# Optimization experiments

Measured on AMD Instinct MI355X. Metric: run time of the kernel, lower is better.

## Reference

```python
import jax, jax.numpy as jnp
import numpy as np

N_NODES = 50000
E0, E1 = 500000, 300000
D = 64  # node_embedding_size == h_feats == edge_embedding_sizes[i]


def _mlp(x, w0, b0, w1, b1, w2, b2):
    # Linear -> ReLU -> Linear -> ReLU -> Linear (nodes_in / edges_in stacks)
    h = jax.nn.relu(x @ w0 + b0)
    h = jax.nn.relu(h @ w1 + b1)
    return h @ w2 + b2


def setup_inputs() -> dict:
    key = jax.random.key(0)
    ks = jax.random.split(key, 32)

    def lin(k, fi, fo):
        return (jax.random.uniform(k, (fi, fo), jnp.float32) - 0.5) * (2.0 / np.sqrt(fi))

    z = lambda n: jnp.zeros((n,), jnp.float32)
    inp = {}
    inp['node_feats'] = jax.random.normal(ks[0], (N_NODES, 32), jnp.float32)
    inp['edge_feats0'] = jax.random.normal(ks[1], (E0, 16), jnp.float32)
    inp['edge_feats1'] = jax.random.normal(ks[2], (E1, 8), jnp.float32)
    # nodes_in MLP
    inp['n_w0'], inp['n_b0'] = lin(ks[3], 32, D), z(D)
    inp['n_w1'], inp['n_b1'] = lin(ks[4], D, D), z(D)
    inp['n_w2'], inp['n_b2'] = lin(ks[5], D, D), z(D)
    # edges_in MLP for edge type 0 (16 -> 64)
    inp['e0_w0'], inp['e0_b0'] = lin(ks[6], 16, D), z(D)
    inp['e0_w1'], inp['e0_b1'] = lin(ks[7], D, D), z(D)
    inp['e0_w2'], inp['e0_b2'] = lin(ks[8], D, D), z(D)
    # edges_in MLP for edge type 1 (8 -> 64)
    inp['e1_w0'], inp['e1_b0'] = lin(ks[9], 8, D), z(D)
    inp['e1_w1'], inp['e1_b1'] = lin(ks[10], D, D), z(D)
    inp['e1_w2'], inp['e1_b2'] = lin(ks[11], D, D), z(D)
    # GraphConv weights
    inp['c1_w'], inp['c1_b'] = lin(ks[12], D, D), z(D)
    inp['c2_w'], inp['c2_b'] = lin(ks[13], D, 1), z(1)
    # edge list (type-0 edges first, then type-1 edges)
    inp['src'] = jax.random.randint(ks[14], (E0 + E1,), 0, N_NODES, dtype=jnp.int32)
    inp['dst'] = jax.random.randint(ks[15], (E0 + E1,), 0, N_NODES, dtype=jnp.int32)
    return inp


def reference(node_feats, edge_feats0, edge_feats1,
              n_w0, n_b0, n_w1, n_b1, n_w2, n_b2,
              e0_w0, e0_b0, e0_w1, e0_b1, e0_w2, e0_b2,
              e1_w0, e1_b0, e1_w1, e1_b1, e1_w2, e1_b2,
              c1_w, c1_b, c2_w, c2_b, src, dst):
    n = node_feats.shape[0]
    # dense embedding stacks
    hn = _mlp(node_feats, n_w0, n_b0, n_w1, n_b1, n_w2, n_b2)          # [N, D]
    he = jnp.concatenate([
        _mlp(edge_feats0, e0_w0, e0_b0, e0_w1, e0_b1, e0_w2, e0_b2),
        _mlp(edge_feats1, e1_w0, e1_b0, e1_w1, e1_b1, e1_w2, e1_b2),
    ], axis=0)                                                          # [E, D]
    # GraphConv symmetric normalization (DGL norm='both'), degrees clamped to 1
    ones = jnp.ones(src.shape, jnp.float32)
    deg_out = jnp.maximum(jax.ops.segment_sum(ones, src, num_segments=n), 1.0)
    deg_in = jnp.maximum(jax.ops.segment_sum(ones, dst, num_segments=n), 1.0)
    norm_e = jax.lax.rsqrt(deg_out[src] * deg_in[dst])[:, None]        # [E, 1]
    # conv1: u_add_v message plus edge embedding, normalized sum aggregation
    msg = (hn[src] + hn[dst] + he) * norm_e                            # [E, D]
    agg1 = jax.ops.segment_sum(msg, dst, num_segments=n)               # [N, D]
    h1 = jax.nn.relu(agg1 @ c1_w + c1_b)                               # [N, D]
    # conv2: standard GraphConv to scalar output
    agg2 = jax.ops.segment_sum(h1[src] * norm_e, dst, num_segments=n)  # [N, D]
    return agg2 @ c2_w + c2_b                                          # [N, 1]
```

## Files before the change

### kernel.cpp

```cpp
#include <hip/hip_runtime.h>

#define N_NODES 50000
#define NE0 500000
#define NE1 300000
#define NE (NE0 + NE1)
#define DD 64
#define ILV 9

typedef __bf16 bf16x8 __attribute__((ext_vector_type(8)));
typedef float f32x4 __attribute__((ext_vector_type(4)));
typedef unsigned short u16x8 __attribute__((ext_vector_type(8)));

__device__ __forceinline__ ushort f2bf(float x) {
  union { __bf16 h; ushort u; } v;
  v.h = (__bf16)x;
  return v.u;
}
__device__ __forceinline__ float bf2f(ushort u) {
  union { unsigned u; float f; } v;
  v.u = ((unsigned)u) << 16;
  return v.f;
}

__device__ __forceinline__ int RP(const int* __restrict__ rowptr,
                                  const int* __restrict__ boff, int i) {
  return (i >= N_NODES) ? NE : rowptr[i] + boff[i >> 8];
}

__global__ void pack_k(const float* __restrict__ w00, const float* __restrict__ w01,
                       const float* __restrict__ w02, const float* __restrict__ w10,
                       const float* __restrict__ w11, const float* __restrict__ w12,
                       const float* __restrict__ w20, const float* __restrict__ w21,
                       const float* __restrict__ w22, ushort* __restrict__ pk) {
  int f = blockIdx.x, l = threadIdx.x;
  int t = f / 20, fl = f % 20;
  int layer, nt, ks;
  if (fl < 4) { layer = 0; nt = fl; ks = 0; }
  else if (fl < 12) { layer = 1; nt = (fl - 4) >> 1; ks = (fl - 4) & 1; }
  else { layer = 2; nt = (fl - 12) >> 1; ks = (fl - 12) & 1; }
  const float* Wt[3][3] = {{w00, w01, w02}, {w10, w11, w12}, {w20, w21, w22}};
  const int K0[3] = {16, 8, 32};
  const float* W = Wt[t][layer];
  int K = (layer == 0) ? K0[t] : 64;
  int g = l >> 4, c = l & 15;
  ushort o[8];
#pragma unroll
  for (int e = 0; e < 8; ++e) {
    int k = ks * 32 + g * 8 + e, n = nt * 16 + c;
    o[e] = f2bf((k < K) ? W[k * DD + n] : 0.f);
  }
  ushort4* d4 = (ushort4*)&pk[(size_t)f * 512 + l * 8];
  d4[0] = make_ushort4(o[0], o[1], o[2], o[3]);
  d4[1] = make_ushort4(o[4], o[5], o[6], o[7]);
}

__device__ __forceinline__ int block_scan_excl(int x, int tid, int* total) {
  int lane = tid & 63, w = tid >> 6;
  int incl = x;
#pragma unroll
  for (int d = 1; d < 64; d <<= 1) {
    int y = __shfl_up(incl, d);
    if (lane >= d) incl += y;
  }
  __shared__ int wsum[4];
  if (lane == 63) wsum[w] = incl;
  __syncthreads();
  int woff = 0;
  if (w > 0) woff = wsum[0];
  if (w > 1) woff += wsum[1];
  if (w > 2) woff += wsum[2];
  *total = wsum[0] + wsum[1] + wsum[2] + wsum[3];
  return woff + incl - x;
}

__global__ __launch_bounds__(256) void scan1_k(const int* __restrict__ cnt,
                                               int* __restrict__ rowptr,
                                               int* __restrict__ bsum) {
  int i = blockIdx.x * 256 + threadIdx.x;
  int x = (i < N_NODES) ? cnt[i] : 0;
  int tot;
  int ex = block_scan_excl(x, threadIdx.x, &tot);
  if (i < N_NODES) rowptr[i] = ex;
  if (threadIdx.x == 0) bsum[blockIdx.x] = tot;
}

__global__ __launch_bounds__(256) void scan2_k(const int* __restrict__ bsum,
                                               int* __restrict__ boff, int nb) {
  int i = threadIdx.x;
  int x = (i < nb) ? bsum[i] : 0;
  int tot;
  int ex = block_scan_excl(x, i, &tot);
  if (i < nb) boff[i] = ex;
}

__global__ void scatter_k(const int* __restrict__ src, const int* __restrict__ dst,
                          const int* __restrict__ rowptr, const int* __restrict__ boff,
                          int* __restrict__ fill, const int* __restrict__ cntO,
                          const int* __restrict__ cntI, int* __restrict__ ceid,
                          int* __restrict__ csrc, float* __restrict__ cnrm) {
  int e = blockIdx.x * 256 + threadIdx.x;
  if (e < NE) {
    int s = src[e], d = dst[e];
    int slot = RP(rowptr, boff, d) + atomicAdd(fill + d, 1);
    ceid[slot] = e;
    csrc[slot] = s;
    cnrm[slot] = rsqrtf((float)max(cntO[s], 1) * (float)max(cntI[d], 1));
  }
}

template <int FIN, bool NODE>
__device__ __forceinline__ void mlp_body(
    ushort (*__restrict__ A)[72], const float* __restrict__ xin,
    const ushort* __restrict__ pk, int pkb, const float* __restrict__ B0,
    const float* __restrict__ B1, const float* __restrict__ B2,
    ushort* __restrict__ msg, float* __restrict__ hn, int r0w, int nR,
    int ebase) {
  const int l = threadIdx.x & 63;
  const int g = l >> 4, c = l & 15;

  {
    int row = l >> 1, half = l & 1;
    int r = r0w + row;
    bool ok = r < nR;
    if (FIN == 32) {
      int cq = half * 16;
#pragma unroll
      for (int q = 0; q < 4; ++q) {
        float4 v = make_float4(0.f, 0.f, 0.f, 0.f);
        if (ok) v = *(const float4*)(xin + (size_t)r * 32 + cq + q * 4);
        *(ushort4*)&A[row][cq + q * 4] =
            make_ushort4(f2bf(v.x), f2bf(v.y), f2bf(v.z), f2bf(v.w));
      }
    } else if (FIN == 16) {
      int cq = half * 8;
#pragma unroll
      for (int q = 0; q < 2; ++q) {
        float4 v = make_float4(0.f, 0.f, 0.f, 0.f);
        if (ok) v = *(const float4*)(xin + (size_t)r * 16 + cq + q * 4);
        *(ushort4*)&A[row][cq + q * 4] =
            make_ushort4(f2bf(v.x), f2bf(v.y), f2bf(v.z), f2bf(v.w));
      }
    } else {
      int cq = half * 4;
      float4 v = make_float4(0.f, 0.f, 0.f, 0.f);
      if (ok) v = *(const float4*)(xin + (size_t)r * 8 + cq);
      *(ushort4*)&A[row][cq] =
          make_ushort4(f2bf(v.x), f2bf(v.y), f2bf(v.z), f2bf(v.w));
    }
  }
  asm volatile("s_waitcnt lgkmcnt(0)" ::: "memory");

  f32x4 acc[2][4];
#pragma unroll
  for (int nt = 0; nt < 4; ++nt) {
    float b = B0[nt * 16 + c];
    acc[0][nt] = f32x4{b, b, b, b};
    acc[1][nt] = acc[0][nt];
  }
  {
    bf16x8 a0 = {}, a1 = {};
    if (g * 8 < FIN) {
      a0 = *(const bf16x8*)&A[c][g * 8];
      a1 = *(const bf16x8*)&A[16 + c][g * 8];
    }
#pragma unroll
    for (int nt = 0; nt < 4; ++nt) {
      bf16x8 bb = *(const bf16x8*)&pk[(size_t)(pkb + nt) * 512 + l * 8];
      acc[0][nt] = __builtin_amdgcn_mfma_f32_16x16x32_bf16(a0, bb, acc[0][nt], 0, 0, 0);
      acc[1][nt] = __builtin_amdgcn_mfma_f32_16x16x32_bf16(a1, bb, acc[1][nt], 0, 0, 0);
    }
  }
#pragma unroll
  for (int t = 0; t < 2; ++t)
#pragma unroll
    for (int nt = 0; nt < 4; ++nt)
#pragma unroll
      for (int r = 0; r < 4; ++r)
        A[t * 16 + g * 4 + r][nt * 16 + c] = f2bf(fmaxf(acc[t][nt][r], 0.f));
  asm volatile("s_waitcnt lgkmcnt(0)" ::: "memory");

#pragma unroll
  for (int nt = 0; nt < 4; ++nt) {
    float b = B1[nt * 16 + c];
    acc[0][nt] = f32x4{b, b, b, b};
    acc[1][nt] = acc[0][nt];
  }
  {
    bf16x8 x00 = *(const bf16x8*)&A[c][g * 8];
    bf16x8 x01 = *(const bf16x8*)&A[c][32 + g * 8];
    bf16x8 x10 = *(const bf16x8*)&A[16 + c][g * 8];
    bf16x8 x11 = *(const bf16x8*)&A[16 + c][32 + g * 8];
#pragma unroll
    for (int nt = 0; nt < 4; ++nt) {
      bf16x8 bb0 = *(const bf16x8*)&pk[(size_t)(pkb + 4 + nt * 2) * 512 + l * 8];
      bf16x8 bb1 = *(const bf16x8*)&pk[(size_t)(pkb + 5 + nt * 2) * 512 + l * 8];
      acc[0][nt] = __builtin_amdgcn_mfma_f32_16x16x32_bf16(x00, bb0, acc[0][nt], 0, 0, 0);
      acc[0][nt] = __builtin_amdgcn_mfma_f32_16x16x32_bf16(x01, bb1, acc[0][nt], 0, 0, 0);
      acc[1][nt] = __builtin_amdgcn_mfma_f32_16x16x32_bf16(x10, bb0, acc[1][nt], 0, 0, 0);
      acc[1][nt] = __builtin_amdgcn_mfma_f32_16x16x32_bf16(x11, bb1, acc[1][nt], 0, 0, 0);
    }
  }
#pragma unroll
  for (int t = 0; t < 2; ++t)
#pragma unroll
    for (int nt = 0; nt < 4; ++nt)
#pragma unroll
      for (int r = 0; r < 4; ++r)
        A[t * 16 + g * 4 + r][nt * 16 + c] = f2bf(fmaxf(acc[t][nt][r], 0.f));
  asm volatile("s_waitcnt lgkmcnt(0)" ::: "memory");

#pragma unroll
  for (int nt = 0; nt < 4; ++nt) {
    float b = B2[nt * 16 + c];
    acc[0][nt] = f32x4{b, b, b, b};
    acc[1][nt] = acc[0][nt];
  }
  {
    bf16x8 x00 = *(const bf16x8*)&A[c][g * 8];
    bf16x8 x01 = *(const bf16x8*)&A[c][32 + g * 8];
    bf16x8 x10 = *(const bf16x8*)&A[16 + c][g * 8];
    bf16x8 x11 = *(const bf16x8*)&A[16 + c][32 + g * 8];
#pragma unroll
    for (int nt = 0; nt < 4; ++nt) {
      bf16x8 bb0 = *(const bf16x8*)&pk[(size_t)(pkb + 12 + nt * 2) * 512 + l * 8];
      bf16x8 bb1 = *(const bf16x8*)&pk[(size_t)(pkb + 13 + nt * 2) * 512 + l * 8];
      acc[0][nt] = __builtin_amdgcn_mfma_f32_16x16x32_bf16(x00, bb0, acc[0][nt], 0, 0, 0);
      acc[0][nt] = __builtin_amdgcn_mfma_f32_16x16x32_bf16(x01, bb1, acc[0][nt], 0, 0, 0);
      acc[1][nt] = __builtin_amdgcn_mfma_f32_16x16x32_bf16(x10, bb0, acc[1][nt], 0, 0, 0);
      acc[1][nt] = __builtin_amdgcn_mfma_f32_16x16x32_bf16(x11, bb1, acc[1][nt], 0, 0, 0);
    }
  }

  if (NODE) {
#pragma unroll
    for (int t = 0; t < 2; ++t)
#pragma unroll
      for (int r = 0; r < 4; ++r) {
        int n = r0w + t * 16 + g * 4 + r;
        if (n < nR) {
          float* hp = hn + (size_t)n * DD + c;
#pragma unroll
          for (int nt = 0; nt < 4; ++nt) hp[nt * 16] = acc[t][nt][r];
        }
      }
  } else {
#pragma unroll
    for (int t = 0; t < 2; ++t)
#pragma unroll
      for (int nt = 0; nt < 4; ++nt)
#pragma unroll
        for (int r = 0; r < 4; ++r)
          A[t * 16 + g * 4 + r][nt * 16 + c] = f2bf(acc[t][nt][r]);
    asm volatile("s_waitcnt lgkmcnt(0)" ::: "memory");
#pragma unroll
    for (int p = 0; p < 4; ++p) {
      int row = p * 8 + (l >> 3);
      int col8 = (l & 7) * 8;
      u16x8 v = *(const u16x8*)&A[row][col8];
      if (r0w + row < nR)
        *(u16x8*)(msg + (size_t)(ebase + r0w + row) * DD + col8) = v;
    }
  }
}

__global__ __launch_bounds__(256, 6) void giant_k(
    const float* __restrict__ nf, const float* __restrict__ ef0,
    const float* __restrict__ ef1, const ushort* __restrict__ pk,
    const float* __restrict__ nb0, const float* __restrict__ nb1,
    const float* __restrict__ nb2, const float* __restrict__ b00,
    const float* __restrict__ b01, const float* __restrict__ b02,
    const float* __restrict__ b10, const float* __restrict__ b11,
    const float* __restrict__ b12, const int* __restrict__ src,
    const int* __restrict__ dst, int* __restrict__ cntO,
    int* __restrict__ cntI, ushort* __restrict__ msg, float* __restrict__ hn,
    int NBc4, int NBn, int NB0v, int NB1v) {
  __shared__ __align__(16) ushort act[4][32][72];
  int bid = blockIdx.x, tid = threadIdx.x, wid = tid >> 6;
  int cnum = bid / ILV;
  if (bid % ILV == ILV - 1) {
    if (cnum < NBc4) {
      int t4 = (cnum * 256 + tid) * 4;
      if (t4 < NE) {
        int4 s4 = *(const int4*)(src + t4);
        int4 d4 = *(const int4*)(dst + t4);
        atomicAdd(cntO + s4.x, 1);
        atomicAdd(cntO + s4.y, 1);
        atomicAdd(cntO + s4.z, 1);
        atomicAdd(cntO + s4.w, 1);
        atomicAdd(cntI + d4.x, 1);
        atomicAdd(cntI + d4.y, 1);
        atomicAdd(cntI + d4.z, 1);
        atomicAdd(cntI + d4.w, 1);
      }
    }
    return;
  }
  int mb = bid - cnum;
  if (mb >= NBn + NB0v + NB1v) return;
  ushort (*A)[72] = act[wid];
  if (mb < NBn) {
    mlp_body<32, true>(A, nf, pk, 40, nb0, nb1, nb2, nullptr, hn,
                       mb * 128 + wid * 32, N_NODES, 0);
  } else if (mb < NBn + NB0v) {
    mlp_body<16, false>(A, ef0, pk, 0, b00, b01, b02, msg, nullptr,
                        (mb - NBn) * 128 + wid * 32, NE0, 0);
  } else {
    mlp_body<8, false>(A, ef1, pk, 20, b10, b11, b12, msg, nullptr,
                       (mb - NBn - NB0v) * 128 + wid * 32, NE1, NE0);
  }
}

__global__ __launch_bounds__(256) void gather_conv1_k(
    const int* __restrict__ rowptr, const int* __restrict__ boff,
    const int* __restrict__ ceid, const int* __restrict__ csrc,
    const float* __restrict__ cnrm, const ushort* __restrict__ msgb,
    const float* __restrict__ hn, const float* __restrict__ c1w,
    const float* __restrict__ c1b, const float* __restrict__ c2w,
    float* __restrict__ sbuf) {
  int w = threadIdx.x >> 6, l = threadIdx.x & 63;
  int g = l >> 4, c = l & 15;
  int n = blockIdx.x * 4 + w;
  if (n >= N_NODES) return;
  int r0 = RP(rowptr, boff, n), r1 = RP(rowptr, boff, n + 1);
  float a0 = 0.f, a1 = 0.f, a2 = 0.f, a3 = 0.f, sn = 0.f;
  for (int j0 = r0; j0 < r1; j0 += 16) {
#pragma unroll
    for (int u = 0; u < 4; ++u) {
      int j = j0 + u * 4 + g;
      bool v = j < r1;
      int js = v ? j : r0;
      int e = ceid[js], s = csrc[js];
      float nm = v ? cnrm[js] : 0.f;
      ushort4 m = *(const ushort4*)(msgb + (size_t)e * DD + c * 4);
      float4 h = *(const float4*)(hn + (size_t)s * DD + c * 4);
      a0 = fmaf(nm, bf2f(m.x) + h.x, a0);
      a1 = fmaf(nm, bf2f(m.y) + h.y, a1);
      a2 = fmaf(nm, bf2f(m.z) + h.z, a2);
      a3 = fmaf(nm, bf2f(m.w) + h.w, a3);
      sn += nm;
    }
  }
  a0 += __shfl_xor(a0, 16); a0 += __shfl_xor(a0, 32);
  a1 += __shfl_xor(a1, 16); a1 += __shfl_xor(a1, 32);
  a2 += __shfl_xor(a2, 16); a2 += __shfl_xor(a2, 32);
  a3 += __shfl_xor(a3, 16); a3 += __shfl_xor(a3, 32);
  sn += __shfl_xor(sn, 16); sn += __shfl_xor(sn, 32);
  float4 hv = *(const float4*)(hn + (size_t)n * DD + c * 4);
  a0 = fmaf(sn, hv.x, a0);
  a1 = fmaf(sn, hv.y, a1);
  a2 = fmaf(sn, hv.z, a2);
  a3 = fmaf(sn, hv.w, a3);
  __shared__ float Asm[4][64];
  if (g == 0) *(float4*)&Asm[w][c * 4] = make_float4(a0, a1, a2, a3);
  float h = c1b[l];
#pragma unroll 8
  for (int k = 0; k < 64; ++k) h = fmaf(Asm[w][k], c1w[k * DD + l], h);
  h = fmaxf(h, 0.f);
  float v = h * c2w[l];
#pragma unroll
  for (int d = 32; d; d >>= 1) v += __shfl_xor(v, d);
  if (l == 0) sbuf[n] = v;
}

__global__ __launch_bounds__(256) void conv2_gather_k(
    const int* __restrict__ rowptr, const int* __restrict__ boff,
    const int* __restrict__ csrc, const float* __restrict__ cnrm,
    const float* __restrict__ sbuf, const float* __restrict__ c2b,
    float* __restrict__ out) {
  int n = blockIdx.x * 16 + (threadIdx.x >> 4);
  int c = threadIdx.x & 15;
  if (n >= N_NODES) return;
  int r0 = RP(rowptr, boff, n), r1 = RP(rowptr, boff, n + 1);
  float a = 0.f;
  for (int j = r0 + c; j < r1; j += 16) a = fmaf(cnrm[j], sbuf[csrc[j]], a);
  a += __shfl_xor(a, 1, 16);
  a += __shfl_xor(a, 2, 16);
  a += __shfl_xor(a, 4, 16);
  a += __shfl_xor(a, 8, 16);
  if (c == 0) out[n] = a + c2b[0];
}

extern "C" void kernel_launch(void* const* d_in, const int* in_sizes, int n_in,
                              void* d_out, int out_size, void* d_ws,
                              size_t ws_size, hipStream_t stream) {
  const float* nf   = (const float*)d_in[0];
  const float* ef0  = (const float*)d_in[1];
  const float* ef1  = (const float*)d_in[2];
  const float* n_w0 = (const float*)d_in[3];  const float* n_b0 = (const float*)d_in[4];
  const float* n_w1 = (const float*)d_in[5];  const float* n_b1 = (const float*)d_in[6];
  const float* n_w2 = (const float*)d_in[7];  const float* n_b2 = (const float*)d_in[8];
  const float* e0w0 = (const float*)d_in[9];  const float* e0b0 = (const float*)d_in[10];
  const float* e0w1 = (const float*)d_in[11]; const float* e0b1 = (const float*)d_in[12];
  const float* e0w2 = (const float*)d_in[13]; const float* e0b2 = (const float*)d_in[14];
  const float* e1w0 = (const float*)d_in[15]; const float* e1b0 = (const float*)d_in[16];
  const float* e1w1 = (const float*)d_in[17]; const float* e1b1 = (const float*)d_in[18];
  const float* e1w2 = (const float*)d_in[19]; const float* e1b2 = (const float*)d_in[20];
  const float* c1w  = (const float*)d_in[21]; const float* c1b  = (const float*)d_in[22];
  const float* c2w  = (const float*)d_in[23]; const float* c2b  = (const float*)d_in[24];
  const int* src = (const int*)d_in[25];
  const int* dst = (const int*)d_in[26];
  float* out = (float*)d_out;
  float* ws = (float*)d_ws;

  float*  hn     = ws;
  float*  sbuf   = ws + 3200000;
  int*    rowptr = (int*)(ws + 3250000);
  int*    cntI   = (int*)(ws + 3300008);
  int*    cntO   = (int*)(ws + 3350008);
  int*    fill   = (int*)(ws + 3400008);
  int*    bsum   = (int*)(ws + 3450008);
  int*    boff   = (int*)(ws + 3450264);
  int*    ceid   = (int*)(ws + 3460000);
  int*    csrc   = (int*)(ws + 4260000);
  float*  cnrm   = ws + 5060000;
  ushort* msg    = (ushort*)(ws + 5860000);
  ushort* pk     = (ushort*)(ws + 31500000);

  const int NB   = (N_NODES + 255) / 256;
  const int NBn  = (N_NODES + 127) / 128;
  const int NB0  = (NE0 + 127) / 128;
  const int NB1  = (NE1 + 127) / 128;
  const int NBc  = (NE + 255) / 256;
  const int NBc4 = (NE + 1023) / 1024;

  const int NMLP = NBn + NB0 + NB1;
  int T = NMLP + NBc4;
  while (T / ILV < NBc4 || T - T / ILV < NMLP) ++T;

  hipMemsetAsync(cntI, 0, (size_t)3 * N_NODES * sizeof(int), stream);
  pack_k<<<60, 64, 0, stream>>>(e0w0, e0w1, e0w2, e1w0, e1w1, e1w2, n_w0,
                                n_w1, n_w2, pk);
  giant_k<<<T, 256, 0, stream>>>(
      nf, ef0, ef1, pk, n_b0, n_b1, n_b2, e0b0, e0b1, e0b2, e1b0, e1b1, e1b2,
      src, dst, cntO, cntI, msg, hn, NBc4, NBn, NB0, NB1);
  scan1_k<<<NB, 256, 0, stream>>>(cntI, rowptr, bsum);
  scan2_k<<<1, 256, 0, stream>>>(bsum, boff, NB);
  scatter_k<<<NBc, 256, 0, stream>>>(src, dst, rowptr, boff, fill, cntO, cntI,
                                     ceid, csrc, cnrm);
  gather_conv1_k<<<(N_NODES + 3) / 4, 256, 0, stream>>>(
      rowptr, boff, ceid, csrc, cnrm, msg, hn, c1w, c1b, c2w, sbuf);
  conv2_gather_k<<<(N_NODES + 15) / 16, 256, 0, stream>>>(
      rowptr, boff, csrc, cnrm, sbuf, c2b, out);
}
```

Baseline: 218.4 us.

## Reuse in-degree atomics as edge ranks, single-pass scan, pack CSR entries as int4

The in-degree atomicAdd return values are stored as per-edge ranks, so the scatter pass no longer needs a second round of fill atomics. The two-level scan is replaced by one pass that claims block bases with a global atomicAdd. Because block order is arbitrary, this yields a valid but non-monotone row layout; row ends are taken as rowptr plus degree. Edge id, source and norm are packed into one int4 per slot so the gathers do one 16-byte load instead of three, at the cost of extra storage and an unused padding word.

```diff
diff --git a/kernel.cpp b/kernel.cpp
--- a/kernel.cpp
+++ b/kernel.cpp
@@ -20,11 +20,6 @@
   union { unsigned u; float f; } v;
   v.u = ((unsigned)u) << 16;
   return v.f;
-}
-
-__device__ __forceinline__ int RP(const int* __restrict__ rowptr,
-                                  const int* __restrict__ boff, int i) {
-  return (i >= N_NODES) ? NE : rowptr[i] + boff[i >> 8];
 }
 
 __global__ void pack_k(const float* __restrict__ w00, const float* __restrict__ w01,
@@ -73,38 +68,36 @@
   return woff + incl - x;
 }
 
-__global__ __launch_bounds__(256) void scan1_k(const int* __restrict__ cnt,
-                                               int* __restrict__ rowptr,
-                                               int* __restrict__ bsum) {
+__global__ __launch_bounds__(256) void scan_k(const int* __restrict__ cnt,
+                                              int* __restrict__ rowptr,
+                                              int* __restrict__ gbase) {
   int i = blockIdx.x * 256 + threadIdx.x;
   int x = (i < N_NODES) ? cnt[i] : 0;
   int tot;
   int ex = block_scan_excl(x, threadIdx.x, &tot);
-  if (i < N_NODES) rowptr[i] = ex;
-  if (threadIdx.x == 0) bsum[blockIdx.x] = tot;
-}
-
-__global__ __launch_bounds__(256) void scan2_k(const int* __restrict__ bsum,
-                                               int* __restrict__ boff, int nb) {
-  int i = threadIdx.x;
-  int x = (i < nb) ? bsum[i] : 0;
-  int tot;
-  int ex = block_scan_excl(x, i, &tot);
-  if (i < nb) boff[i] = ex;
+  __shared__ int base;
+  if (threadIdx.x == 0) base = atomicAdd(gbase, tot);
+  __syncthreads();
+  if (i < N_NODES) rowptr[i] = base + ex;
 }
 
 __global__ void scatter_k(const int* __restrict__ src, const int* __restrict__ dst,
-                          const int* __restrict__ rowptr, const int* __restrict__ boff,
-                          int* __restrict__ fill, const int* __restrict__ cntO,
-                          const int* __restrict__ cntI, int* __restrict__ ceid,
-                          int* __restrict__ csrc, float* __restrict__ cnrm) {
+                          const int* __restrict__ rowptr,
+                          const int* __restrict__ rank,
+                          const int* __restrict__ cntO,
+                          const int* __restrict__ cntI,
+                          int4* __restrict__ cslot) {
   int e = blockIdx.x * 256 + threadIdx.x;
   if (e < NE) {
     int s = src[e], d = dst[e];
-    int slot = RP(rowptr, boff, d) + atomicAdd(fill + d, 1);
-    ceid[slot] = e;
-    csrc[slot] = s;
-    cnrm[slot] = rsqrtf((float)max(cntO[s], 1) * (float)max(cntI[d], 1));
+    int slot = rowptr[d] + rank[e];
+    float nm = rsqrtf((float)max(cntO[s], 1) * (float)max(cntI[d], 1));
+    int4 q;
+    q.x = e;
+    q.y = s;
+    q.z = __float_as_int(nm);
+    q.w = 0;
+    cslot[slot] = q;
   }
 }
 
@@ -272,7 +265,8 @@
     const float* __restrict__ b10, const float* __restrict__ b11,
     const float* __restrict__ b12, const int* __restrict__ src,
     const int* __restrict__ dst, int* __restrict__ cntO,
-    int* __restrict__ cntI, ushort* __restrict__ msg, float* __restrict__ hn,
+    int* __restrict__ cntI, int* __restrict__ rank,
+    ushort* __restrict__ msg, float* __restrict__ hn,
     int NBc4, int NBn, int NB0v, int NB1v) {
   __shared__ __align__(16) ushort act[4][32][72];
   int bid = blockIdx.x, tid = threadIdx.x, wid = tid >> 6;
@@ -287,10 +281,12 @@
         atomicAdd(cntO + s4.y, 1);
         atomicAdd(cntO + s4.z, 1);
         atomicAdd(cntO + s4.w, 1);
-        atomicAdd(cntI + d4.x, 1);
-        atomicAdd(cntI + d4.y, 1);
-        atomicAdd(cntI + d4.z, 1);
-        atomicAdd(cntI + d4.w, 1);
+        int4 r;
+        r.x = atomicAdd(cntI + d4.x, 1);
+        r.y = atomicAdd(cntI + d4.y, 1);
+        r.z = atomicAdd(cntI + d4.z, 1);
+        r.w = atomicAdd(cntI + d4.w, 1);
+        *(int4*)(rank + t4) = r;
       }
     }
     return;
@@ -311,9 +307,8 @@
 }
 
 __global__ __launch_bounds__(256) void gather_conv1_k(
-    const int* __restrict__ rowptr, const int* __restrict__ boff,
-    const int* __restrict__ ceid, const int* __restrict__ csrc,
-    const float* __restrict__ cnrm, const ushort* __restrict__ msgb,
+    const int* __restrict__ rowptr, const int* __restrict__ deg,
+    const int4* __restrict__ cslot, const ushort* __restrict__ msgb,
     const float* __restrict__ hn, const float* __restrict__ c1w,
     const float* __restrict__ c1b, const float* __restrict__ c2w,
     float* __restrict__ sbuf) {
@@ -321,7 +316,7 @@
   int g = l >> 4, c = l & 15;
   int n = blockIdx.x * 4 + w;
   if (n >= N_NODES) return;
-  int r0 = RP(rowptr, boff, n), r1 = RP(rowptr, boff, n + 1);
+  int r0 = rowptr[n], r1 = r0 + deg[n];
   float a0 = 0.f, a1 = 0.f, a2 = 0.f, a3 = 0.f, sn = 0.f;
   for (int j0 = r0; j0 < r1; j0 += 16) {
 #pragma unroll
@@ -329,8 +324,9 @@
       int j = j0 + u * 4 + g;
       bool v = j < r1;
       int js = v ? j : r0;
-      int e = ceid[js], s = csrc[js];
-      float nm = v ? cnrm[js] : 0.f;
+      int4 q = cslot[js];
+      int e = q.x, s = q.y;
+      float nm = v ? __int_as_float(q.z) : 0.f;
       ushort4 m = *(const ushort4*)(msgb + (size_t)e * DD + c * 4);
       float4 h = *(const float4*)(hn + (size_t)s * DD + c * 4);
       a0 = fmaf(nm, bf2f(m.x) + h.x, a0);
@@ -363,16 +359,18 @@
 }
 
 __global__ __launch_bounds__(256) void conv2_gather_k(
-    const int* __restrict__ rowptr, const int* __restrict__ boff,
-    const int* __restrict__ csrc, const float* __restrict__ cnrm,
-    const float* __restrict__ sbuf, const float* __restrict__ c2b,
-    float* __restrict__ out) {
+    const int* __restrict__ rowptr, const int* __restrict__ deg,
+    const int4* __restrict__ cslot, const float* __restrict__ sbuf,
+    const float* __restrict__ c2b, float* __restrict__ out) {
   int n = blockIdx.x * 16 + (threadIdx.x >> 4);
   int c = threadIdx.x & 15;
   if (n >= N_NODES) return;
-  int r0 = RP(rowptr, boff, n), r1 = RP(rowptr, boff, n + 1);
+  int r0 = rowptr[n], r1 = r0 + deg[n];
   float a = 0.f;
-  for (int j = r0 + c; j < r1; j += 16) a = fmaf(cnrm[j], sbuf[csrc[j]], a);
+  for (int j = r0 + c; j < r1; j += 16) {
+    int4 q = cslot[j];
+    a = fmaf(__int_as_float(q.z), sbuf[q.y], a);
+  }
   a += __shfl_xor(a, 1, 16);
   a += __shfl_xor(a, 2, 16);
   a += __shfl_xor(a, 4, 16);
@@ -407,14 +405,11 @@
   int*    rowptr = (int*)(ws + 3250000);
   int*    cntI   = (int*)(ws + 3300008);
   int*    cntO   = (int*)(ws + 3350008);
-  int*    fill   = (int*)(ws + 3400008);
-  int*    bsum   = (int*)(ws + 3450008);
-  int*    boff   = (int*)(ws + 3450264);
-  int*    ceid   = (int*)(ws + 3460000);
-  int*    csrc   = (int*)(ws + 4260000);
-  float*  cnrm   = ws + 5060000;
-  ushort* msg    = (ushort*)(ws + 5860000);
-  ushort* pk     = (ushort*)(ws + 31500000);
+  int*    gbase  = (int*)(ws + 3400008);
+  int*    rank   = (int*)(ws + 3410000);
+  int4*   cslot  = (int4*)(ws + 4210000);
+  ushort* msg    = (ushort*)(ws + 7410000);
+  ushort* pk     = (ushort*)(ws + 33010000);
 
   const int NB   = (N_NODES + 255) / 256;
   const int NBn  = (N_NODES + 127) / 128;
@@ -427,18 +422,17 @@
   int T = NMLP + NBc4;
   while (T / ILV < NBc4 || T - T / ILV < NMLP) ++T;
 
-  hipMemsetAsync(cntI, 0, (size_t)3 * N_NODES * sizeof(int), stream);
+  hipMemsetAsync(cntI, 0, (size_t)100016 * sizeof(int), stream);
   pack_k<<<60, 64, 0, stream>>>(e0w0, e0w1, e0w2, e1w0, e1w1, e1w2, n_w0,
                                 n_w1, n_w2, pk);
   giant_k<<<T, 256, 0, stream>>>(
       nf, ef0, ef1, pk, n_b0, n_b1, n_b2, e0b0, e0b1, e0b2, e1b0, e1b1, e1b2,
-      src, dst, cntO, cntI, msg, hn, NBc4, NBn, NB0, NB1);
-  scan1_k<<<NB, 256, 0, stream>>>(cntI, rowptr, bsum);
-  scan2_k<<<1, 256, 0, stream>>>(bsum, boff, NB);
-  scatter_k<<<NBc, 256, 0, stream>>>(src, dst, rowptr, boff, fill, cntO, cntI,
-                                     ceid, csrc, cnrm);
+      src, dst, cntO, cntI, rank, msg, hn, NBc4, NBn, NB0, NB1);
+  scan_k<<<NB, 256, 0, stream>>>(cntI, rowptr, gbase);
+  scatter_k<<<NBc, 256, 0, stream>>>(src, dst, rowptr, rank, cntO, cntI,
+                                     cslot);
   gather_conv1_k<<<(N_NODES + 3) / 4, 256, 0, stream>>>(
-      rowptr, boff, ceid, csrc, cnrm, msg, hn, c1w, c1b, c2w, sbuf);
+      rowptr, cntI, cslot, msg, hn, c1w, c1b, c2w, sbuf);
   conv2_gather_k<<<(N_NODES + 15) / 16, 256, 0, stream>>>(
-      rowptr, boff, csrc, cnrm, sbuf, c2b, out);
-}
+      rowptr, cntI, cslot, sbuf, c2b, out);
+}
```

New measurement: 196.2 us. 1.11x faster.
